# Kernel optimization log

Measured on AMD Instinct MI355X. Metric: run time of the kernel, lower is better.

Reference implementation:

```python
import jax, jax.numpy as jnp
import numpy as np

LEAKY_SLOPE = 0.01

def bilinear_interpolate(grid, coords):
    # grid: [H, W, C]; coords: [N, 2] in [0,1] (x, y order as in torch code)
    H = grid.shape[0] - 1
    W = grid.shape[1] - 1
    fx = coords[:, 0] * W
    fy = coords[:, 1] * H
    x0 = fx.astype(jnp.int32)
    y0 = fy.astype(jnp.int32)
    xf = jnp.mod(fx, 1.0)
    yf = jnp.mod(fy, 1.0)
    x1 = jnp.minimum(x0 + 1, W)
    y1 = jnp.minimum(y0 + 1, H)
    tl = grid[y0, x0]  # [N, C]
    tr = grid[y0, x1]
    bl = grid[y1, x0]
    br = grid[y1, x1]
    xf = xf[:, None]
    yf = yf[:, None]
    top = (1.0 - xf) * tl + xf * tr
    bot = (1.0 - xf) * bl + xf * br
    return (1.0 - yf) * top + yf * bot


def setup_inputs() -> dict:
    key = jax.random.key(0)
    ks = jax.random.split(key, 10)
    N = 2097152
    pos = jax.random.uniform(ks[0], (N, 2), dtype=jnp.float32)
    dir = jax.random.uniform(ks[1], (N, 2), dtype=jnp.float32)
    pos_grid = jax.random.normal(ks[2], (256, 256, 3), dtype=jnp.float32) * 10.0
    dir_grid = jax.random.normal(ks[3], (256, 256, 3), dtype=jnp.float32) * 10.0
    # Linear layers: PyTorch default init U(-1/sqrt(fan_in), 1/sqrt(fan_in))
    def linear(kw, kb, fan_in, fan_out):
        bound = 1.0 / np.sqrt(fan_in)
        W = jax.random.uniform(kw, (fan_out, fan_in), minval=-bound, maxval=bound, dtype=jnp.float32)
        b = jax.random.uniform(kb, (fan_out,), minval=-bound, maxval=bound, dtype=jnp.float32)
        return W, b
    W1, b1 = linear(ks[4], ks[5], 6, 64)
    W2, b2 = linear(ks[6], ks[7], 64, 64)
    W3, b3 = linear(ks[8], ks[9], 64, 1)
    return {"pos": pos, "dir": dir, "pos_grid": pos_grid, "dir_grid": dir_grid,
            "W1": W1, "b1": b1, "W2": W2, "b2": b2, "W3": W3, "b3": b3}


def reference(pos, dir, pos_grid, dir_grid, W1, b1, W2, b2, W3, b3):
    pos_feat = jax.lax.stop_gradient(bilinear_interpolate(pos_grid, pos))  # .detach() in torch
    dir_feat = jax.lax.stop_gradient(bilinear_interpolate(dir_grid, dir))
    x = jnp.concatenate([pos_feat, dir_feat], axis=1)  # [N, 6]
    x = jax.nn.leaky_relu(x @ W1.T + b1, LEAKY_SLOPE)
    x = jax.nn.leaky_relu(x @ W2.T + b2, LEAKY_SLOPE)
    return jax.nn.sigmoid(x @ W3.T + b3)  # [N, 1]
```

## Files before the change

kernel.cpp:

```cpp
#include <hip/hip_runtime.h>
#include <hip/hip_bf16.h>
#include <math.h>


#define NTHREADS 256
#define NB 4

typedef __attribute__((ext_vector_type(4))) short s16x4;
typedef __attribute__((ext_vector_type(4))) float f32x4;
typedef __attribute__((ext_vector_type(4))) int i32x4;
typedef __attribute__((ext_vector_type(2))) int i32x2;

static __device__ __forceinline__ short f2bf(float f) {
    return __builtin_bit_cast(short, __float2bfloat16(f));
}
static __device__ __forceinline__ int pk2(float lo, float hi) {
    unsigned short l = (unsigned short)f2bf(lo);
    unsigned short h = (unsigned short)f2bf(hi);
    return (int)(((unsigned int)h << 16) | (unsigned int)l);
}
static __device__ __forceinline__ float bflo(int u) {
    return __builtin_bit_cast(float, u << 16);
}
static __device__ __forceinline__ float bfhi(int u) {
    return __builtin_bit_cast(float, (int)(u & 0xffff0000));
}

__global__ __launch_bounds__(256) void make_patches(
    const float* __restrict__ gP, const float* __restrict__ gD,
    int* __restrict__ outP, int* __restrict__ outD) {
    int gid = blockIdx.x * 256 + threadIdx.x;
    const float* g = (gid < 65536) ? gP : gD;
    int* po = (gid < 65536) ? outP : outD;
    int id = gid & 65535;
    int y0 = id >> 8, x0 = id & 255;
    int x1 = min(x0 + 1, 255), y1 = min(y0 + 1, 255);
    const float* tl = g + (y0 * 256 + x0) * 3;
    const float* tr = g + (y0 * 256 + x1) * 3;
    const float* bl = g + (y1 * 256 + x0) * 3;
    const float* br = g + (y1 * 256 + x1) * 3;
    i32x4 u0;
    i32x2 u1;
    u0[0] = pk2(tl[0], bl[0]);
    u0[1] = pk2(tl[1], bl[1]);
    u0[2] = pk2(tl[2], bl[2]);
    u0[3] = pk2(tr[0], br[0]);
    u1[0] = pk2(tr[1], br[1]);
    u1[1] = pk2(tr[2], br[2]);
    *(i32x4*)(po + id * 8) = u0;
    *(i32x2*)(po + id * 8 + 4) = u1;
}

static __device__ __forceinline__ void patch_issue(
    const int* __restrict__ tab, float px, float py, int* P, float& xf,
    float& yf) {
    float fx = px * 255.0f;
    float fy = py * 255.0f;
    int x0 = (int)fx;
    int y0 = (int)fy;
    xf = fx - floorf(fx);
    yf = fy - floorf(fy);
    int idx = (y0 << 8) | x0;
    i32x4 a = *(const i32x4*)(tab + idx * 8);
    i32x2 b = *(const i32x2*)(tab + idx * 8 + 4);
    P[0] = a[0]; P[1] = a[1]; P[2] = a[2];
    P[3] = a[3]; P[4] = b[0]; P[5] = b[1];
}

static __device__ __forceinline__ void patch_lerp(const int* P, float xf,
                                                  float yf, float* f) {
#pragma unroll
    for (int ch = 0; ch < 3; ++ch) {
        float tl = bflo(P[ch]), bl = bfhi(P[ch]);
        float tr = bflo(P[ch + 3]), br = bfhi(P[ch + 3]);
        float top = fmaf(xf, tr - tl, tl);
        float bot = fmaf(xf, br - bl, bl);
        f[ch] = fmaf(yf, bot - top, top);
    }
}

__global__ __launch_bounds__(NTHREADS, 3) void mlp_mfma_kernel(
    const float* __restrict__ pos, const float* __restrict__ dir,
    const int* __restrict__ patP, const int* __restrict__ patD,
    const float* __restrict__ W1, const float* __restrict__ b1,
    const float* __restrict__ W2, const float* __restrict__ b2,
    const float* __restrict__ W3, const float* __restrict__ b3,
    float* __restrict__ out) {
    __shared__ int lds_F[4 * 2 * 64 * 4];

    const int w = threadIdx.x >> 6;
    const int lane = threadIdx.x & 63;
    const int c = lane & 15;
    const int q = lane >> 4;

    int* FB = lds_F + w * (2 * 64 * 4);

    s16x4 A1f[4];
#pragma unroll
    for (int mt = 0; mt < 4; ++mt) {
        int f = mt * 16 + c;
        s16x4 t;
#pragma unroll
        for (int j = 0; j < 4; ++j) {
            int k = q * 4 + j;
            float v = 0.0f;
            if (k < 6) v = W1[f * 6 + k];
            else if (k == 6) v = b1[f];
            t[j] = f2bf(v);
        }
        A1f[mt] = t;
    }
    s16x4 A2f[4][4];
#pragma unroll
    for (int kt = 0; kt < 4; ++kt)
#pragma unroll
        for (int mt = 0; mt < 4; ++mt) {
            int n2 = mt * 16 + c;
            int k0 = kt * 16 + q * 4;
            s16x4 t;
#pragma unroll
            for (int j = 0; j < 4; ++j) t[j] = f2bf(W2[n2 * 64 + k0 + j]);
            A2f[kt][mt] = t;
        }
    f32x4 ci[4], w3q[4];
#pragma unroll
    for (int mt = 0; mt < 4; ++mt)
#pragma unroll
        for (int r = 0; r < 4; ++r) {
            ci[mt][r] = b2[mt * 16 + q * 4 + r];
            w3q[mt][r] = W3[mt * 16 + q * 4 + r];
        }
    const float b3s = b3[0];
    const int dbias = pk2(1.0f, 0.0f);
    const f32x4 zacc = {0.f, 0.f, 0.f, 0.f};

    const long wave_global = (long)blockIdx.x * 4 + w;
    const long base0 = wave_global * (64L * NB);
    const float2* pos2 = (const float2*)pos;
    const float2* dir2 = (const float2*)dir;

    float2 cp1, cd1;
    {
        float2 c0p = pos2[base0 + lane], c0d = dir2[base0 + lane];
        cp1 = pos2[base0 + 64 + lane];
        cd1 = dir2[base0 + 64 + lane];
        int P0_[12];
        float fr0[4];
        patch_issue(patP, c0p.x, c0p.y, P0_, fr0[0], fr0[1]);
        patch_issue(patD, c0d.x, c0d.y, P0_ + 6, fr0[2], fr0[3]);
        float feat[6];
        patch_lerp(P0_, fr0[0], fr0[1], feat);
        patch_lerp(P0_ + 6, fr0[2], fr0[3], feat + 3);
        i32x4 dv;
        dv[0] = pk2(feat[0], feat[1]);
        dv[1] = pk2(feat[2], feat[3]);
        dv[2] = pk2(feat[4], feat[5]);
        dv[3] = dbias;
        *(i32x4*)(FB + lane * 4) = dv;
    }

#pragma unroll 1
    for (int ib = 0; ib < NB; ++ib) {
        const long base = base0 + ib * 64;
        const int cur = ib & 1;

        int PB[12];
        float frB[4];
        patch_issue(patP, cp1.x, cp1.y, PB, frB[0], frB[1]);
        patch_issue(patD, cd1.x, cd1.y, PB + 6, frB[2], frB[3]);

        {
            int mb = min(ib + 2, NB - 1);
            cp1 = pos2[base0 + mb * 64 + lane];
            cd1 = dir2[base0 + mb * 64 + lane];
        }

        float s[4];
#pragma unroll
        for (int t = 0; t < 4; ++t) {
            i32x2 bi = *(const i32x2*)(FB + cur * 256 + (t * 16 + c) * 4 +
                                       (q & 1) * 2);
            s16x4 bfeat = __builtin_bit_cast(s16x4, bi);

            f32x4 a1[4];
#pragma unroll
            for (int mt = 0; mt < 4; ++mt)
                a1[mt] = __builtin_amdgcn_mfma_f32_16x16x16bf16_1k(
                    A1f[mt], bfeat, zacc, 0, 0, 0);

            s16x4 bh[4];
#pragma unroll
            for (int kt = 0; kt < 4; ++kt) {
                s16x4 hv;
#pragma unroll
                for (int r = 0; r < 4; ++r) {
                    float x = a1[kt][r];
                    hv[r] = f2bf(fmaxf(x, 0.01f * x));
                }
                bh[kt] = hv;
            }

            f32x4 a2[4];
#pragma unroll
            for (int mt = 0; mt < 4; ++mt) a2[mt] = ci[mt];
#pragma unroll
            for (int kt = 0; kt < 4; ++kt)
#pragma unroll
                for (int mt = 0; mt < 4; ++mt)
                    a2[mt] = __builtin_amdgcn_mfma_f32_16x16x16bf16_1k(
                        A2f[kt][mt], bh[kt], a2[mt], 0, 0, 0);

            float tt = 0.0f;
#pragma unroll
            for (int mt = 0; mt < 4; ++mt)
#pragma unroll
                for (int r = 0; r < 4; ++r) {
                    float x = a2[mt][r];
                    x = fmaxf(x, 0.01f * x);
                    tt = fmaf(x, w3q[mt][r], tt);
                }
            tt += __shfl_xor(tt, 16, 64);
            tt += __shfl_xor(tt, 32, 64);
            s[t] = tt;
        }

        float sa = (q & 1) ? s[1] : s[0];
        float sb = (q & 1) ? s[3] : s[2];
        float v = (q & 2) ? sb : sa;
        v += b3s;
        v = 1.0f / (1.0f + __expf(-v));
        out[base + q * 16 + c] = v;

        {
            float feat[6];
            patch_lerp(PB, frB[0], frB[1], feat);
            patch_lerp(PB + 6, frB[2], frB[3], feat + 3);
            i32x4 dv;
            dv[0] = pk2(feat[0], feat[1]);
            dv[1] = pk2(feat[2], feat[3]);
            dv[2] = pk2(feat[4], feat[5]);
            dv[3] = dbias;
            *(i32x4*)(FB + (cur ^ 1) * 256 + lane * 4) = dv;
        }
    }
}

extern "C" void kernel_launch(void* const* d_in, const int* in_sizes, int n_in,
                              void* d_out, int out_size, void* d_ws,
                              size_t ws_size, hipStream_t stream) {
    const float* pos = (const float*)d_in[0];
    const float* dir = (const float*)d_in[1];
    const float* pos_grid = (const float*)d_in[2];
    const float* dir_grid = (const float*)d_in[3];
    const float* W1 = (const float*)d_in[4];
    const float* b1 = (const float*)d_in[5];
    const float* W2 = (const float*)d_in[6];
    const float* b2 = (const float*)d_in[7];
    const float* W3 = (const float*)d_in[8];
    const float* b3 = (const float*)d_in[9];
    float* out = (float*)d_out;

    int* patP = (int*)d_ws;
    int* patD = patP + 65536 * 8;

    make_patches<<<512, 256, 0, stream>>>(pos_grid, dir_grid, patP, patD);

    const int n = in_sizes[0] / 2;
    const int batches = n / 64;
    const int waves = batches / NB;
    const int blocks = waves / 4;

    mlp_mfma_kernel<<<blocks, NTHREADS, 0, stream>>>(
        pos, dir, patP, patD, W1, b1, W2, b2, W3, b3, out);
}
```

Before: 157.7 us.

## Move b2/W3 constants to LDS, rewrite leaky ReLU algebraically, raise occupancy

```diff
diff --git a/kernel.cpp b/kernel.cpp
--- a/kernel.cpp
+++ b/kernel.cpp
@@ -24,6 +24,10 @@
 }
 static __device__ __forceinline__ float bfhi(int u) {
     return __builtin_bit_cast(float, (int)(u & 0xffff0000));
+}
+static __device__ __forceinline__ int opaq(int x) {
+    asm volatile("" : "+v"(x));
+    return x;
 }
 
 __global__ __launch_bounds__(256) void make_patches(
@@ -79,7 +83,7 @@
     }
 }
 
-__global__ __launch_bounds__(NTHREADS, 3) void mlp_mfma_kernel(
+__global__ __launch_bounds__(NTHREADS, 4) void mlp_mfma_kernel(
     const float* __restrict__ pos, const float* __restrict__ dir,
     const int* __restrict__ patP, const int* __restrict__ patD,
     const float* __restrict__ W1, const float* __restrict__ b1,
@@ -87,11 +91,17 @@
     const float* __restrict__ W3, const float* __restrict__ b3,
     float* __restrict__ out) {
     __shared__ int lds_F[4 * 2 * 64 * 4];
-
-    const int w = threadIdx.x >> 6;
-    const int lane = threadIdx.x & 63;
+    __shared__ __align__(16) float cw[128];
+
+    const int tid = threadIdx.x;
+    if (tid < 128) cw[tid] = (tid < 64) ? b2[tid] : W3[tid - 64];
+    __syncthreads();
+
+    const int w = tid >> 6;
+    const int lane = tid & 63;
     const int c = lane & 15;
     const int q = lane >> 4;
+    const int q4 = q * 4;
 
     int* FB = lds_F + w * (2 * 64 * 4);
 
@@ -102,7 +112,7 @@
         s16x4 t;
 #pragma unroll
         for (int j = 0; j < 4; ++j) {
-            int k = q * 4 + j;
+            int k = q4 + j;
             float v = 0.0f;
             if (k < 6) v = W1[f * 6 + k];
             else if (k == 6) v = b1[f];
@@ -116,19 +126,11 @@
 #pragma unroll
         for (int mt = 0; mt < 4; ++mt) {
             int n2 = mt * 16 + c;
-            int k0 = kt * 16 + q * 4;
+            int k0 = kt * 16 + q4;
             s16x4 t;
 #pragma unroll
             for (int j = 0; j < 4; ++j) t[j] = f2bf(W2[n2 * 64 + k0 + j]);
             A2f[kt][mt] = t;
-        }
-    f32x4 ci[4], w3q[4];
-#pragma unroll
-    for (int mt = 0; mt < 4; ++mt)
-#pragma unroll
-        for (int r = 0; r < 4; ++r) {
-            ci[mt][r] = b2[mt * 16 + q * 4 + r];
-            w3q[mt][r] = W3[mt * 16 + q * 4 + r];
         }
     const float b3s = b3[0];
     const int dbias = pk2(1.0f, 0.0f);
@@ -201,8 +203,12 @@
             }
 
             f32x4 a2[4];
-#pragma unroll
-            for (int mt = 0; mt < 4; ++mt) a2[mt] = ci[mt];
+            {
+                const float* cwb = cw + opaq(q4);
+#pragma unroll
+                for (int mt = 0; mt < 4; ++mt)
+                    a2[mt] = *(const f32x4*)(cwb + mt * 16);
+            }
 #pragma unroll
             for (int kt = 0; kt < 4; ++kt)
 #pragma unroll
@@ -210,15 +216,19 @@
                     a2[mt] = __builtin_amdgcn_mfma_f32_16x16x16bf16_1k(
                         A2f[kt][mt], bh[kt], a2[mt], 0, 0, 0);
 
-            float tt = 0.0f;
-#pragma unroll
-            for (int mt = 0; mt < 4; ++mt)
+            float tx = 0.0f, ta = 0.0f;
+            const float* cww = cw + opaq(64 + q4);
+#pragma unroll
+            for (int mt = 0; mt < 4; ++mt) {
+                const f32x4 wv = *(const f32x4*)(cww + mt * 16);
 #pragma unroll
                 for (int r = 0; r < 4; ++r) {
                     float x = a2[mt][r];
-                    x = fmaxf(x, 0.01f * x);
-                    tt = fmaf(x, w3q[mt][r], tt);
+                    tx = fmaf(x, wv[r], tx);
+                    ta = fmaf(__builtin_fabsf(x), wv[r], ta);
                 }
+            }
+            float tt = fmaf(0.505f, tx, 0.495f * ta);
             tt += __shfl_xor(tt, 16, 64);
             tt += __shfl_xor(tt, 32, 64);
             s[t] = tt;
```

New measurement: 153.9 us. -2.4%, faster.
